# Performance work log

Measured on AMD Instinct MI355X. Metric: run time of the kernel, lower is better.

## Reference

```python
import jax, jax.numpy as jnp
import numpy as np

DT = 0.5  # integration time step (init_kwargs dt)


def setup_inputs() -> dict:
    key = jax.random.key(0)
    ks = jax.random.split(key, 6)
    B, T, I, H, O = 64, 1024, 64, 512, 64
    g, g_in = 1.0, 1.0
    return {
        "input": jax.random.normal(ks[0], (B, T, I), dtype=jnp.float32),
        "wi": jax.random.normal(ks[1], (I, H), dtype=jnp.float32) * (g_in / np.sqrt(H)),
        "wrec": jax.random.normal(ks[2], (H, H), dtype=jnp.float32) * (g / np.sqrt(H)),
        "wo": jax.random.normal(ks[3], (H, O), dtype=jnp.float32) * (1.0 / np.sqrt(H)),
        "brec": jnp.zeros((H,), dtype=jnp.float32),
        "h0": jax.random.uniform(ks[4], (H,), dtype=jnp.float32, minval=-1.0, maxval=1.0),
    }


def reference(input, wi, wrec, wo, brec, h0):
    # ML_RNN=True, nonlinearity=tanh, readout=id, noise_std=0.0
    B = input.shape[0]
    # Precompute input projection for all timesteps: [B, T, H]
    xproj = jnp.einsum("bti,ih->bth", input, wi) + brec
    h_init = jnp.broadcast_to(h0, (B, h0.shape[0]))

    def step(h, x_t):
        rec = jnp.tanh(h @ wrec.T + x_t)  # [B, H]
        h_new = (1.0 - DT) * h + DT * rec
        return h_new, h_new

    # scan over time: xproj transposed to [T, B, H]
    _, hs = jax.lax.scan(step, h_init, jnp.swapaxes(xproj, 0, 1))
    hs = jnp.swapaxes(hs, 0, 1)  # [B, T, H]
    output = jnp.einsum("bth,ho->bto", hs, wo)  # readout nonlinearity = id
    return output
```

## Files before the change

### kernel.cpp

```cpp
#include <hip/hip_runtime.h>

#define Tn 1024
#define Bn 64
#define In_ 64
#define Hn 512
#define On 64
#define DTC 0.5f

typedef __attribute__((ext_vector_type(8))) short short8;
typedef __attribute__((ext_vector_type(4))) short short4v;
typedef __attribute__((ext_vector_type(4))) float floatx4;
typedef unsigned long long u64;

__device__ __forceinline__ float bf2f(unsigned short u){
  union{unsigned int i; float f;} v; v.i = ((unsigned int)u)<<16; return v.f;
}
__device__ __forceinline__ unsigned short f2bf(float f){
  union{float f; unsigned int i;} v; v.f=f;
  unsigned int x=v.i;
  return (unsigned short)((x + 0x7fffu + ((x>>16)&1u))>>16);
}
__device__ __forceinline__ short8 cvt8(const float* p){
  short8 v;
  #pragma unroll
  for (int e=0;e<8;e++) v[e] = (short)f2bf(p[e]);
  return v;
}
__device__ __forceinline__ void barrier_lds(){
  asm volatile("s_waitcnt lgkmcnt(0)\n\ts_barrier" ::: "memory");
}

__global__ __launch_bounds__(256,2) void xproj_kernel(
    const float* __restrict__ inp, const float* __restrict__ wi,
    const float* __restrict__ brec, unsigned short* __restrict__ xp)
{
  const int t = blockIdx.x, tid = threadIdx.x;
  const int wv = tid>>6, lane = tid&63, col = lane&15, quad = lane>>4;
  __shared__ __align__(16) unsigned short inA[64*80];
  {
    int r = tid>>2, i0 = (tid&3)*16;
    const float* src = inp + ((size_t)r*Tn + t)*In_ + i0;
    unsigned short tmp[16];
    #pragma unroll
    for (int q=0;q<16;q++) tmp[q] = f2bf(src[q]);
    *(short8*)&inA[r*80 + i0]     = *(short8*)&tmp[0];
    *(short8*)&inA[r*80 + i0 + 8] = *(short8*)&tmp[8];
  }
  const int wnb = wv*128;
  short8 bw[8][2];
  float brecv[8];
  #pragma unroll
  for (int nt=0;nt<8;nt++){
    int j = wnb + nt*16 + col;
    brecv[nt] = brec[j];
    #pragma unroll
    for (int ks=0;ks<2;ks++){
      float tmp[8];
      #pragma unroll
      for (int e=0;e<8;e++) tmp[e] = wi[(size_t)(ks*32 + quad*8 + e)*Hn + j];
      bw[nt][ks] = cvt8(tmp);
    }
  }
  __syncthreads();
  floatx4 acc[4][8];
  #pragma unroll
  for (int mt=0;mt<4;mt++)
    #pragma unroll
    for (int nt=0;nt<8;nt++) acc[mt][nt] = (floatx4){0.f,0.f,0.f,0.f};
  #pragma unroll
  for (int ks=0;ks<2;ks++)
    #pragma unroll
    for (int mt=0;mt<4;mt++){
      short8 ar = *(const short8*)&inA[(mt*16+col)*80 + ks*32 + quad*8];
      #pragma unroll
      for (int nt=0;nt<8;nt++)
        acc[mt][nt] = __builtin_amdgcn_mfma_f32_16x16x32_bf16(ar, bw[nt][ks], acc[mt][nt],0,0,0);
    }
  #pragma unroll
  for (int mt=0;mt<4;mt++)
    #pragma unroll
    for (int nt=0;nt<8;nt++)
      #pragma unroll
      for (int r=0;r<4;r++){
        int b = mt*16 + quad*4 + r;
        int j = wnb + nt*16 + col;
        xp[((size_t)t*Bn + b)*Hn + j] = f2bf(acc[mt][nt][r] + brecv[nt]);
      }
}

__global__ __launch_bounds__(256,1) void wrec_pack(
    const float* __restrict__ wrec, unsigned short* __restrict__ wrecB)
{
  int gl = blockIdx.x*256 + threadIdx.x;
  int fi = gl>>6, lane = gl&63;
  int gmt = fi>>1, ksx = fi&1;
  int j = gmt*16 + (lane&15);
  int k = 320 + ksx*32 + (lane>>4)*8;
  short8 v = cvt8(wrec + (size_t)j*Hn + k);
  *(short8*)(wrecB + (size_t)gl*8) = v;
}

__global__ __launch_bounds__(512,2) void rnn_scan(
    const float* __restrict__ wrec, const float* __restrict__ h0,
    const unsigned short* xp,
    const unsigned short* __restrict__ wrecB,
    unsigned short* hs)
{
  const int tid  = threadIdx.x;
  const int g    = blockIdx.x;
  const int wv   = tid >> 6;
  const int lane = tid & 63;
  const int col  = lane & 15;
  const int quad = lane >> 4;
  const int wbase = wv*64;

  __shared__ __align__(16) unsigned short wrecL[65536];
  __shared__ __align__(16) unsigned short hA[8192];

  short8 awr[4][10];
  #pragma unroll
  for (int mt=0;mt<4;mt++)
    #pragma unroll
    for (int ks=0;ks<10;ks++){
      int j = wbase + mt*16 + col;
      int k = ks*32 + quad*8;
      awr[mt][ks] = cvt8(wrec + (size_t)j*Hn + k);
    }
  #pragma unroll
  for (int mt=0;mt<4;mt++)
    #pragma unroll
    for (int ks2=0;ks2<4;ks2++){
      int j = wbase + mt*16 + col;
      int k = 384 + ks2*32 + quad*8;
      short8 v = cvt8(wrec + (size_t)j*Hn + k);
      *(short8*)&wrecL[(((wv*4+mt)*4 + ks2))*512 + lane*8] = v;
    }
  for (int idx = tid; idx < 16*Hn; idx += 512){
    int b = idx >> 9, k = idx & 511;
    hA[(((k>>5)*64 + ((k>>3)&3)*16 + b))*8 + (k&7)] = f2bf(h0[k]);
  }
  float hm[4][4];
  #pragma unroll
  for (int mt=0;mt<4;mt++)
    #pragma unroll
    for (int r=0;r<4;r++) hm[mt][r] = h0[wbase + mt*16 + quad*4 + r];

  floatx4 acc[4];
  #pragma unroll
  for (int mt=0;mt<4;mt++) acc[mt] = (floatx4){0.f,0.f,0.f,0.f};

  const size_t row = (size_t)(g*16 + col);
  __syncthreads();

  for (int t = 0; t < Tn; t++){
    short8 wst[4];
    u64 xv[4];
    #pragma unroll
    for (int mt=0;mt<4;mt++)
      wst[mt] = *(const short8*)(wrecB + (size_t)(((wv*4+mt)*2 + 0)*64 + lane)*8);
    #pragma unroll
    for (int mt=0;mt<4;mt++)
      xv[mt] = *(const u64*)(xp + (size_t)t*(Bn*Hn) + row*Hn + wbase + mt*16 + quad*4);

    #pragma unroll
    for (int ks=0;ks<10;ks++){
      short8 hb = *(const short8*)&hA[ks*512 + lane*8];
      #pragma unroll
      for (int mt=0;mt<4;mt++)
        acc[mt] = __builtin_amdgcn_mfma_f32_16x16x32_bf16(awr[mt][ks], hb, acc[mt],0,0,0);
    }
    {
      short8 hb = *(const short8*)&hA[10*512 + lane*8];
      #pragma unroll
      for (int mt=0;mt<4;mt++)
        acc[mt] = __builtin_amdgcn_mfma_f32_16x16x32_bf16(wst[mt], hb, acc[mt],0,0,0);
    }
    #pragma unroll
    for (int mt=0;mt<4;mt++)
      wst[mt] = *(const short8*)(wrecB + (size_t)(((wv*4+mt)*2 + 1)*64 + lane)*8);
    #pragma unroll
    for (int ks2=0;ks2<4;ks2++){
      short8 hb = *(const short8*)&hA[(12+ks2)*512 + lane*8];
      #pragma unroll
      for (int mt=0;mt<4;mt++){
        short8 aw = *(const short8*)&wrecL[(((wv*4+mt)*4 + ks2))*512 + lane*8];
        acc[mt] = __builtin_amdgcn_mfma_f32_16x16x32_bf16(aw, hb, acc[mt],0,0,0);
      }
    }
    {
      short8 hb = *(const short8*)&hA[11*512 + lane*8];
      #pragma unroll
      for (int mt=0;mt<4;mt++)
        acc[mt] = __builtin_amdgcn_mfma_f32_16x16x32_bf16(wst[mt], hb, acc[mt],0,0,0);
    }

    barrier_lds();

    #pragma unroll
    for (int mt=0;mt<4;mt++){
      u64 x = xv[mt];
      unsigned short hv[4];
      #pragma unroll
      for (int r=0;r<4;r++){
        float pre = acc[mt][r] + bf2f((unsigned short)(x >> (16*r)));
        float e2x = __expf(2.0f*pre);
        float rec = 1.0f - 2.0f/(e2x + 1.0f);
        float hn  = (1.0f-DTC)*hm[mt][r] + DTC*rec;
        hm[mt][r] = hn;
        hv[r] = f2bf(hn);
      }
      int j4 = wbase + mt*16 + quad*4;
      *(short4v*)&hA[(((j4>>5)*64 + ((j4>>3)&3)*16 + col))*8 + (j4&7)] = *(short4v*)hv;
      u64 pk = (u64)hv[0] | ((u64)hv[1]<<16) | ((u64)hv[2]<<32) | ((u64)hv[3]<<48);
      __builtin_nontemporal_store(pk, (u64*)(hs + (size_t)t*(Bn*Hn) + row*Hn + j4));
      acc[mt] = (floatx4){0.f,0.f,0.f,0.f};
    }
    barrier_lds();
  }
}

__global__ __launch_bounds__(256,1) void out_gemm(
    const unsigned short* __restrict__ hs,
    const float* __restrict__ wo,
    float* __restrict__ out)
{
  const int tid = threadIdx.x, bid = blockIdx.x;
  const int wv = tid >> 6, lane = tid & 63, col = lane & 15, quad = lane >> 4;
  const int m0 = bid*64;
  __shared__ __align__(16) unsigned short hsA[64][520];

  for (int c = tid; c < 64*64; c += 256){
    int r = c >> 6, cc = (c & 63)*8;
    *(short8*)&hsA[r][cc] = *(const short8*)(hs + (size_t)(m0 + r)*Hn + cc);
  }
  short8 boh[16], bol[16];
  #pragma unroll
  for (int kk = 0; kk < 16; kk++){
    float tmp[8];
    #pragma unroll
    for (int e = 0; e < 8; e++) tmp[e] = wo[(size_t)(kk*32 + quad*8 + e)*On + wv*16 + col];
    #pragma unroll
    for (int e = 0; e < 8; e++){
      unsigned short h = f2bf(tmp[e]);
      boh[kk][e] = (short)h;
      bol[kk][e] = (short)f2bf(tmp[e] - bf2f(h));
    }
  }
  __syncthreads();

  floatx4 acc[4];
  #pragma unroll
  for (int ms=0;ms<4;ms++) acc[ms] = (floatx4){0.f,0.f,0.f,0.f};
  #pragma unroll
  for (int kk = 0; kk < 16; kk++){
    int k = kk*32 + quad*8;
    #pragma unroll
    for (int ms = 0; ms < 4; ms++){
      short8 a = *(const short8*)&hsA[ms*16 + col][k];
      acc[ms] = __builtin_amdgcn_mfma_f32_16x16x32_bf16(a, boh[kk], acc[ms], 0,0,0);
      acc[ms] = __builtin_amdgcn_mfma_f32_16x16x32_bf16(a, bol[kk], acc[ms], 0,0,0);
    }
  }
  #pragma unroll
  for (int ms = 0; ms < 4; ms++)
    #pragma unroll
    for (int r = 0; r < 4; r++){
      int m = m0 + ms*16 + quad*4 + r;
      int b = m & 63, tt = m >> 6;
      out[((size_t)b*Tn + tt)*On + wv*16 + col] = acc[ms][r];
    }
}

extern "C" void kernel_launch(void* const* d_in, const int* in_sizes, int n_in,
                              void* d_out, int out_size, void* d_ws, size_t ws_size,
                              hipStream_t stream){
  const float* inp  = (const float*)d_in[0];
  const float* wi   = (const float*)d_in[1];
  const float* wrec = (const float*)d_in[2];
  const float* wo   = (const float*)d_in[3];
  const float* brec = (const float*)d_in[4];
  const float* h0   = (const float*)d_in[5];
  float* out = (float*)d_out;

  char* ws = (char*)d_ws;
  unsigned short* hs = (unsigned short*)ws;
  unsigned short* xp = (unsigned short*)(ws + 65536);
  unsigned short* wrecB = (unsigned short*)(ws + (size_t)Tn*Bn*Hn*2 + 65536);

  xproj_kernel<<<Tn, 256, 0, stream>>>(inp, wi, brec, xp);
  wrec_pack  <<<16, 256, 0, stream>>>(wrec, wrecB);
  rnn_scan   <<<4, 512, 0, stream>>>(wrec, h0, xp, wrecB, hs);
  out_gemm   <<<(Bn*Tn)/64, 256, 0, stream>>>(hs, wo, out);
}
```

Baseline: 3.488 ms.

## Double-buffer hidden state in LDS and rebalance recurrent-weight storage split

Double-buffers the bf16 hidden-state tile in LDS so each timestep needs only one barrier instead of two. Fully pre-packs the recurrent weights into MFMA fragment layout in a wider pack kernel, then splits them 9 slices in registers, 4 streamed from global per step, and 3 in LDS. Also simplifies the tanh update with a hardware reciprocal and packed bf16 conversion instruction, and hoists address arithmetic out of the time loop. The aim is to shorten the serial per-step latency of the scan. The cost is more global weight traffic per step, and the approximate reciprocal may change accuracy slightly.

```diff
diff --git a/kernel.cpp b/kernel.cpp
--- a/kernel.cpp
+++ b/kernel.cpp
@@ -8,7 +8,6 @@
 #define DTC 0.5f
 
 typedef __attribute__((ext_vector_type(8))) short short8;
-typedef __attribute__((ext_vector_type(4))) short short4v;
 typedef __attribute__((ext_vector_type(4))) float floatx4;
 typedef unsigned long long u64;
 
@@ -25,6 +24,14 @@
   #pragma unroll
   for (int e=0;e<8;e++) v[e] = (short)f2bf(p[e]);
   return v;
+}
+__device__ __forceinline__ unsigned int cvtpk_bf16(float a, float b){
+  unsigned int r;
+  asm("v_cvt_pk_bf16_f32 %0, %1, %2" : "=v"(r) : "v"(a), "v"(b));
+  return r;
+}
+__device__ __forceinline__ float fast_rcp(float x){
+  float r; asm("v_rcp_f32 %0, %1" : "=v"(r) : "v"(x)); return r;
 }
 __device__ __forceinline__ void barrier_lds(){
   asm volatile("s_waitcnt lgkmcnt(0)\n\ts_barrier" ::: "memory");
@@ -93,15 +100,15 @@
 {
   int gl = blockIdx.x*256 + threadIdx.x;
   int fi = gl>>6, lane = gl&63;
-  int gmt = fi>>1, ksx = fi&1;
-  int j = gmt*16 + (lane&15);
-  int k = 320 + ksx*32 + (lane>>4)*8;
+  int jt = fi>>4, ks = fi&15;
+  int j = jt*16 + (lane&15);
+  int k = ks*32 + (lane>>4)*8;
   short8 v = cvt8(wrec + (size_t)j*Hn + k);
   *(short8*)(wrecB + (size_t)gl*8) = v;
 }
 
 __global__ __launch_bounds__(512,2) void rnn_scan(
-    const float* __restrict__ wrec, const float* __restrict__ h0,
+    const float* __restrict__ h0,
     const unsigned short* xp,
     const unsigned short* __restrict__ wrecB,
     unsigned short* hs)
@@ -114,27 +121,28 @@
   const int quad = lane >> 4;
   const int wbase = wv*64;
 
-  __shared__ __align__(16) unsigned short wrecL[65536];
-  __shared__ __align__(16) unsigned short hA[8192];
-
-  short8 awr[4][10];
-  #pragma unroll
-  for (int mt=0;mt<4;mt++)
-    #pragma unroll
-    for (int ks=0;ks<10;ks++){
-      int j = wbase + mt*16 + col;
-      int k = ks*32 + quad*8;
-      awr[mt][ks] = cvt8(wrec + (size_t)j*Hn + k);
-    }
-  #pragma unroll
-  for (int mt=0;mt<4;mt++)
-    #pragma unroll
-    for (int ks2=0;ks2<4;ks2++){
-      int j = wbase + mt*16 + col;
-      int k = 384 + ks2*32 + quad*8;
-      short8 v = cvt8(wrec + (size_t)j*Hn + k);
-      *(short8*)&wrecL[(((wv*4+mt)*4 + ks2))*512 + lane*8] = v;
-    }
+  __shared__ __align__(16) unsigned short wrecL[32*3*512];
+  __shared__ __align__(16) unsigned short hA[2*8192];
+
+  const unsigned short* wb9[4];
+  #pragma unroll
+  for (int mt=0;mt<4;mt++)
+    wb9[mt] = wrecB + ((size_t)((wv*4+mt)*16 + 9))*512 + lane*8;
+
+  short8 awr[4][9];
+  #pragma unroll
+  for (int mt=0;mt<4;mt++)
+    #pragma unroll
+    for (int ks=0;ks<9;ks++)
+      awr[mt][ks] = *(const short8*)(wb9[mt] + (ks-9)*512);
+
+  #pragma unroll
+  for (int mt=0;mt<4;mt++)
+    #pragma unroll
+    for (int ls=0;ls<3;ls++)
+      *(short8*)&wrecL[((wv*4+mt)*3+ls)*512 + lane*8] =
+          *(const short8*)(wb9[mt] + (4+ls)*512);
+
   for (int idx = tid; idx < 16*Hn; idx += 512){
     int b = idx >> 9, k = idx & 511;
     hA[(((k>>5)*64 + ((k>>3)&3)*16 + b))*8 + (k&7)] = f2bf(h0[k]);
@@ -149,73 +157,103 @@
   #pragma unroll
   for (int mt=0;mt<4;mt++) acc[mt] = (floatx4){0.f,0.f,0.f,0.f};
 
-  const size_t row = (size_t)(g*16 + col);
+  const int row = g*16 + col;
+  int xoff[4], woff[4];
+  #pragma unroll
+  for (int mt=0;mt<4;mt++){
+    int j4 = wbase + mt*16 + quad*4;
+    xoff[mt] = row*Hn + j4;
+    woff[mt] = (((j4>>5)*64 + ((j4>>3)&3)*16 + col))*8 + (j4&7);
+  }
+  const unsigned short* xq = xp;
+  unsigned short* hq = hs;
+  int hoff = 0;
+
   __syncthreads();
 
   for (int t = 0; t < Tn; t++){
-    short8 wst[4];
+    short8 wst0[4], wst1[4];
     u64 xv[4];
     #pragma unroll
-    for (int mt=0;mt<4;mt++)
-      wst[mt] = *(const short8*)(wrecB + (size_t)(((wv*4+mt)*2 + 0)*64 + lane)*8);
-    #pragma unroll
-    for (int mt=0;mt<4;mt++)
-      xv[mt] = *(const u64*)(xp + (size_t)t*(Bn*Hn) + row*Hn + wbase + mt*16 + quad*4);
-
-    #pragma unroll
-    for (int ks=0;ks<10;ks++){
-      short8 hb = *(const short8*)&hA[ks*512 + lane*8];
+    for (int mt=0;mt<4;mt++) wst0[mt] = *(const short8*)(wb9[mt]);
+    #pragma unroll
+    for (int mt=0;mt<4;mt++) wst1[mt] = *(const short8*)(wb9[mt] + 512);
+    #pragma unroll
+    for (int mt=0;mt<4;mt++) xv[mt] = *(const u64*)(xq + xoff[mt]);
+
+    const unsigned short* hc = hA + hoff + lane*8;
+
+    #pragma unroll
+    for (int ks=0;ks<9;ks++){
+      short8 hb = *(const short8*)(hc + ks*512);
       #pragma unroll
       for (int mt=0;mt<4;mt++)
         acc[mt] = __builtin_amdgcn_mfma_f32_16x16x32_bf16(awr[mt][ks], hb, acc[mt],0,0,0);
     }
     {
-      short8 hb = *(const short8*)&hA[10*512 + lane*8];
-      #pragma unroll
-      for (int mt=0;mt<4;mt++)
-        acc[mt] = __builtin_amdgcn_mfma_f32_16x16x32_bf16(wst[mt], hb, acc[mt],0,0,0);
-    }
-    #pragma unroll
-    for (int mt=0;mt<4;mt++)
-      wst[mt] = *(const short8*)(wrecB + (size_t)(((wv*4+mt)*2 + 1)*64 + lane)*8);
-    #pragma unroll
-    for (int ks2=0;ks2<4;ks2++){
-      short8 hb = *(const short8*)&hA[(12+ks2)*512 + lane*8];
+      short8 hb = *(const short8*)(hc + 9*512);
+      #pragma unroll
+      for (int mt=0;mt<4;mt++)
+        acc[mt] = __builtin_amdgcn_mfma_f32_16x16x32_bf16(wst0[mt], hb, acc[mt],0,0,0);
+    }
+    #pragma unroll
+    for (int mt=0;mt<4;mt++) wst0[mt] = *(const short8*)(wb9[mt] + 2*512);
+    {
+      short8 hb = *(const short8*)(hc + 10*512);
+      #pragma unroll
+      for (int mt=0;mt<4;mt++)
+        acc[mt] = __builtin_amdgcn_mfma_f32_16x16x32_bf16(wst1[mt], hb, acc[mt],0,0,0);
+    }
+    #pragma unroll
+    for (int mt=0;mt<4;mt++) wst1[mt] = *(const short8*)(wb9[mt] + 3*512);
+    #pragma unroll
+    for (int ls=0;ls<3;ls++){
+      short8 hb = *(const short8*)(hc + (13+ls)*512);
       #pragma unroll
       for (int mt=0;mt<4;mt++){
-        short8 aw = *(const short8*)&wrecL[(((wv*4+mt)*4 + ks2))*512 + lane*8];
+        short8 aw = *(const short8*)&wrecL[((wv*4+mt)*3+ls)*512 + lane*8];
         acc[mt] = __builtin_amdgcn_mfma_f32_16x16x32_bf16(aw, hb, acc[mt],0,0,0);
       }
     }
     {
-      short8 hb = *(const short8*)&hA[11*512 + lane*8];
-      #pragma unroll
-      for (int mt=0;mt<4;mt++)
-        acc[mt] = __builtin_amdgcn_mfma_f32_16x16x32_bf16(wst[mt], hb, acc[mt],0,0,0);
-    }
-
-    barrier_lds();
-
+      short8 hb = *(const short8*)(hc + 11*512);
+      #pragma unroll
+      for (int mt=0;mt<4;mt++)
+        acc[mt] = __builtin_amdgcn_mfma_f32_16x16x32_bf16(wst0[mt], hb, acc[mt],0,0,0);
+    }
+    {
+      short8 hb = *(const short8*)(hc + 12*512);
+      #pragma unroll
+      for (int mt=0;mt<4;mt++)
+        acc[mt] = __builtin_amdgcn_mfma_f32_16x16x32_bf16(wst1[mt], hb, acc[mt],0,0,0);
+    }
+
+    unsigned short* hw = hA + (hoff ^ 8192);
     #pragma unroll
     for (int mt=0;mt<4;mt++){
       u64 x = xv[mt];
-      unsigned short hv[4];
+      float hn[4];
       #pragma unroll
       for (int r=0;r<4;r++){
         float pre = acc[mt][r] + bf2f((unsigned short)(x >> (16*r)));
-        float e2x = __expf(2.0f*pre);
-        float rec = 1.0f - 2.0f/(e2x + 1.0f);
-        float hn  = (1.0f-DTC)*hm[mt][r] + DTC*rec;
-        hm[mt][r] = hn;
-        hv[r] = f2bf(hn);
+        float e   = __expf(2.0f*pre);
+        float rc  = fast_rcp(e + 1.0f);
+        float v   = __builtin_fmaf(0.5f, hm[mt][r], 0.5f) - rc;
+        hm[mt][r] = v;
+        hn[r] = v;
       }
-      int j4 = wbase + mt*16 + quad*4;
-      *(short4v*)&hA[(((j4>>5)*64 + ((j4>>3)&3)*16 + col))*8 + (j4&7)] = *(short4v*)hv;
-      u64 pk = (u64)hv[0] | ((u64)hv[1]<<16) | ((u64)hv[2]<<32) | ((u64)hv[3]<<48);
-      __builtin_nontemporal_store(pk, (u64*)(hs + (size_t)t*(Bn*Hn) + row*Hn + j4));
+      unsigned int lo = cvtpk_bf16(hn[0], hn[1]);
+      unsigned int hi = cvtpk_bf16(hn[2], hn[3]);
+      uint2 w; w.x = lo; w.y = hi;
+      *(uint2*)&hw[woff[mt]] = w;
+      u64 pk = (u64)lo | ((u64)hi << 32);
+      __builtin_nontemporal_store(pk, (u64*)(hq + xoff[mt]));
       acc[mt] = (floatx4){0.f,0.f,0.f,0.f};
     }
     barrier_lds();
+    hoff ^= 8192;
+    xq += Bn*Hn;
+    hq += Bn*Hn;
   }
 }
 
@@ -288,7 +326,7 @@
   unsigned short* wrecB = (unsigned short*)(ws + (size_t)Tn*Bn*Hn*2 + 65536);
 
   xproj_kernel<<<Tn, 256, 0, stream>>>(inp, wi, brec, xp);
-  wrec_pack  <<<16, 256, 0, stream>>>(wrec, wrecB);
-  rnn_scan   <<<4, 512, 0, stream>>>(wrec, h0, xp, wrecB, hs);
+  wrec_pack  <<<128, 256, 0, stream>>>(wrec, wrecB);
+  rnn_scan   <<<4, 512, 0, stream>>>(h0, xp, wrecB, hs);
   out_gemm   <<<(Bn*Tn)/64, 256, 0, stream>>>(hs, wo, out);
 }
```

Result: slower. 3.717 ms (+6.5%).
